# Optimization experiments

Measured on AMD Instinct MI355X. Metric: run time of the kernel, lower is better.

Reference implementation:

```python
import jax, jax.numpy as jnp
import numpy as np

INV_SQRT3 = 1.0 / np.sqrt(3.0)


def setup_inputs() -> dict:
    key = jax.random.key(0)
    ks = jax.random.split(key, 7)
    N = 100000
    M0, M1 = 128, 64  # multiplicities of 0e and 1o irreps in in1 / out
    data_in1 = jax.random.normal(ks[0], (N, M0 + 3 * M1), jnp.float32)  # [N, 320]
    data_in2 = jax.random.normal(ks[1], (N, 1 + 3), jnp.float32)        # [N, 4] = 1x0e + 1x1o
    # e3nn-style path weights, standard normal init (path_normalization='none')
    W00 = jax.random.normal(ks[2], (M0, 1, M0), jnp.float32)  # 0e x 0e -> 0e
    W01 = jax.random.normal(ks[3], (M0, 1, M1), jnp.float32)  # 0e x 1o -> 1o
    W10 = jax.random.normal(ks[4], (M1, 1, M1), jnp.float32)  # 1o x 0e -> 1o
    W11 = jax.random.normal(ks[5], (M1, 1, M0), jnp.float32)  # 1o x 1o -> 0e
    # fan_in of the scalar output slice = 128*1 (0e x 0e) + 64*1 (1o x 1o) = 192
    sqrt_k = 1.0 / np.sqrt(M0 + M1)
    bias = jax.random.uniform(ks[6], (M0,), jnp.float32, -sqrt_k, sqrt_k)
    return {"data_in1": data_in1, "data_in2": data_in2,
            "W00": W00, "W01": W01, "W10": W10, "W11": W11, "bias": bias}


def reference(data_in1, data_in2, W00, W01, W10, W11, bias):
    M0, M1 = W00.shape[0], W10.shape[0]
    N = data_in1.shape[0]
    s1 = data_in1[:, :M0]                      # [N, 128]  scalars 0e
    v1 = data_in1[:, M0:].reshape(N, M1, 3)    # [N, 64, 3] vectors 1o
    s2 = data_in2[:, :1]                       # [N, 1]    scalar attr
    v2 = data_in2[:, 1:].reshape(N, 1, 3)      # [N, 1, 3] vector attr
    # CG paths (component irrep-normalization, path_normalization='none'):
    # wigner-3j folded analytically; net per-path coefs are 1,1,1,1/sqrt(3)
    out0 = jnp.einsum('nu,nv,uvw->nw', s1, s2, W00)                       # 0e x 0e -> 0e
    out0 = out0 + INV_SQRT3 * jnp.einsum('nui,nvi,uvw->nw', v1, v2, W11)  # 1o x 1o -> 0e
    outv = jnp.einsum('nu,nvk,uvw->nwk', s1, v2, W01)                     # 0e x 1o -> 1o
    outv = outv + jnp.einsum('nuk,nv,uvw->nwk', v1, s2, W10)              # 1o x 0e -> 1o
    # indexed bias add: bias_idx selects the l=0 output slice [0:M0]
    out0 = out0 + bias
    return jnp.concatenate([out0, outv.reshape(N, M1 * 3)], axis=1)      # [N, 320]
```

## Files before the change

kernel.cpp:

```cpp
#include <hip/hip_runtime.h>

typedef __bf16 bf16_8 __attribute__((ext_vector_type(8)));
typedef float  f32x4  __attribute__((ext_vector_type(4)));
typedef float  f32x3  __attribute__((ext_vector_type(3), aligned(4)));

#define INV_SQRT3f 0.57735026918962576f


__global__ void tp_convert_weights(
    const float* __restrict__ W00, const float* __restrict__ W01,
    const float* __restrict__ W10, const float* __restrict__ W11,
    __bf16* __restrict__ ws)
{
    const int chunk = blockIdx.x * blockDim.x + threadIdx.x;
    bf16_8 v;
    if (chunk < 2048) {
        const int c = chunk >> 4, q = chunk & 15;
#pragma unroll
        for (int j = 0; j < 8; ++j) v[j] = (__bf16)W00[(q * 8 + j) * 128 + c];
        *(bf16_8*)(ws + (c * 16 + (q ^ (c & 15))) * 8) = v;
    } else if (chunk < 3072) {
        const int idx = chunk - 2048;
        const int c = idx >> 4, q = idx & 15;
#pragma unroll
        for (int j = 0; j < 8; ++j) v[j] = (__bf16)W01[(q * 8 + j) * 64 + c];
        *(bf16_8*)(ws + 16384 + (c * 16 + (q ^ (c & 15))) * 8) = v;
    } else if (chunk < 4096) {
        const int idx = chunk - 3072;
        const int c = idx >> 3, q = idx & 7;
#pragma unroll
        for (int j = 0; j < 8; ++j) v[j] = (__bf16)W11[(q * 8 + j) * 128 + c];
        *(bf16_8*)(ws + 24576 + (c * 8 + (q ^ (c & 7))) * 8) = v;
    } else if (chunk < 4608) {
        const int idx = chunk - 4096;
        const int c = idx >> 3, q = idx & 7;
#pragma unroll
        for (int j = 0; j < 8; ++j) v[j] = (__bf16)W10[(q * 8 + j) * 64 + c];
        *(bf16_8*)(ws + 32768 + idx * 8) = v;
    }
}

__global__ __launch_bounds__(512, 4) void tp_main_kernel(
    const float* __restrict__ din1, const float* __restrict__ din2,
    const __bf16* __restrict__ wsw, const float* __restrict__ bias,
    float* __restrict__ out, int N, int nstrips)
{
    __shared__ __attribute__((aligned(16))) __bf16 smem[32768];
    const __bf16* sw00 = smem;
    const __bf16* sw01 = smem + 16384;
    const __bf16* sw11 = smem + 24576;

    const int tid = threadIdx.x;

    {
        f32x4* d = (f32x4*)smem;
        const f32x4* s = (const f32x4*)wsw;
#pragma unroll
        for (int i = 0; i < 8; ++i)
            d[tid + 512 * i] = s[tid + 512 * i];
    }
    __syncthreads();

    const int wid = (blockIdx.x << 3) + (tid >> 6);
    if (wid < nstrips) {
        const int lane = tid & 63;
        const int mh   = lane & 15;
        const int kq   = lane >> 4;

        int row = wid * 16 + mh;  if (row >= N) row = N - 1;
        const float* __restrict__ r1 = din1 + row * 320;
        const f32x4 d2 = *(const f32x4*)(din2 + row * 4);
        const float s2 = d2.x;

        const __bf16* __restrict__ w10g = wsw + 32768;

        f32x4 accA[8];
        f32x4 accV[3][4];
#pragma unroll
        for (int i = 0; i < 8; ++i) accA[i] = (f32x4)0.0f;
#pragma unroll
        for (int k = 0; k < 3; ++k)
#pragma unroll
            for (int i = 0; i < 4; ++i) accV[k][i] = (f32x4)0.0f;

#pragma unroll
        for (int s = 0; s < 4; ++s) {
            const int off = 32 * s + 8 * kq;
            f32x4 x0 = *(const f32x4*)(r1 + off);
            f32x4 x1 = *(const f32x4*)(r1 + off + 4);
            float xx[8] = {x0.x, x0.y, x0.z, x0.w, x1.x, x1.y, x1.z, x1.w};
            bf16_8 as2, av0, av1, av2;
#pragma unroll
            for (int j = 0; j < 8; ++j) {
                as2[j] = (__bf16)(s2   * xx[j]);
                av0[j] = (__bf16)(d2.y * xx[j]);
                av1[j] = (__bf16)(d2.z * xx[j]);
                av2[j] = (__bf16)(d2.w * xx[j]);
            }
            const int q = 4 * s + kq;
#pragma unroll
            for (int nt = 0; nt < 8; ++nt) {
                const int c = nt * 16 + mh;
                bf16_8 b = *(const bf16_8*)(sw00 + (c * 16 + (q ^ mh)) * 8);
                accA[nt] = __builtin_amdgcn_mfma_f32_16x16x32_bf16(as2, b, accA[nt], 0, 0, 0);
            }
#pragma unroll
            for (int nt = 0; nt < 4; ++nt) {
                const int c = nt * 16 + mh;
                bf16_8 b = *(const bf16_8*)(sw01 + (c * 16 + (q ^ mh)) * 8);
                accV[0][nt] = __builtin_amdgcn_mfma_f32_16x16x32_bf16(av0, b, accV[0][nt], 0, 0, 0);
                accV[1][nt] = __builtin_amdgcn_mfma_f32_16x16x32_bf16(av1, b, accV[1][nt], 0, 0, 0);
                accV[2][nt] = __builtin_amdgcn_mfma_f32_16x16x32_bf16(av2, b, accV[2][nt], 0, 0, 0);
            }
        }

#pragma unroll
        for (int s = 0; s < 2; ++s) {
            const int voff = 128 + 96 * s + 24 * kq;
            float b24[24];
#pragma unroll
            for (int qq = 0; qq < 6; ++qq) {
                f32x4 t4 = *(const f32x4*)(r1 + voff + 4 * qq);
                b24[4 * qq]     = t4.x; b24[4 * qq + 1] = t4.y;
                b24[4 * qq + 2] = t4.z; b24[4 * qq + 3] = t4.w;
            }
            bf16_8 at, ac0, ac1, ac2;
#pragma unroll
            for (int j = 0; j < 8; ++j) {
                const float e0 = b24[3 * j], e1 = b24[3 * j + 1], e2 = b24[3 * j + 2];
                at[j]  = (__bf16)(INV_SQRT3f * (e0 * d2.y + e1 * d2.z + e2 * d2.w));
                ac0[j] = (__bf16)(s2 * e0);
                ac1[j] = (__bf16)(s2 * e1);
                ac2[j] = (__bf16)(s2 * e2);
            }
            const int q = 4 * s + kq;
#pragma unroll
            for (int nt = 0; nt < 8; ++nt) {
                const int c = nt * 16 + mh;
                bf16_8 b = *(const bf16_8*)(sw11 + (c * 8 + (q ^ (mh & 7))) * 8);
                accA[nt] = __builtin_amdgcn_mfma_f32_16x16x32_bf16(at, b, accA[nt], 0, 0, 0);
            }
#pragma unroll
            for (int nt = 0; nt < 4; ++nt) {
                const int c = nt * 16 + mh;
                bf16_8 b = *(const bf16_8*)(w10g + (c * 8 + q) * 8);
                accV[0][nt] = __builtin_amdgcn_mfma_f32_16x16x32_bf16(ac0, b, accV[0][nt], 0, 0, 0);
                accV[1][nt] = __builtin_amdgcn_mfma_f32_16x16x32_bf16(ac1, b, accV[1][nt], 0, 0, 0);
                accV[2][nt] = __builtin_amdgcn_mfma_f32_16x16x32_bf16(ac2, b, accV[2][nt], 0, 0, 0);
            }
        }

        const int rowg0 = wid * 16 + 4 * kq;
#pragma unroll
        for (int nt = 0; nt < 8; ++nt) {
            const float bi = bias[nt * 16 + mh];
#pragma unroll
            for (int r = 0; r < 4; ++r) {
                const int rowg = rowg0 + r;
                if (rowg < N) out[rowg * 320 + nt * 16 + mh] = accA[nt][r] + bi;
            }
        }
#pragma unroll
        for (int r = 0; r < 4; ++r) {
            const int rowg = rowg0 + r;
            if (rowg < N) {
#pragma unroll
                for (int nt = 0; nt < 4; ++nt) {
                    const int w = nt * 16 + mh;
                    f32x3 o;
                    o.x = accV[0][nt][r];
                    o.y = accV[1][nt][r];
                    o.z = accV[2][nt][r];
                    *(f32x3*)(out + rowg * 320 + 128 + 3 * w) = o;
                }
            }
        }
    }
}

extern "C" void kernel_launch(void* const* d_in, const int* in_sizes, int n_in,
                              void* d_out, int out_size, void* d_ws, size_t ws_size,
                              hipStream_t stream)
{
    const float* din1 = (const float*)d_in[0];
    const float* din2 = (const float*)d_in[1];
    const float* W00  = (const float*)d_in[2];
    const float* W01  = (const float*)d_in[3];
    const float* W10  = (const float*)d_in[4];
    const float* W11  = (const float*)d_in[5];
    const float* bias = (const float*)d_in[6];
    float* outp = (float*)d_out;
    __bf16* ws = (__bf16*)d_ws;

    const int N = in_sizes[0] / 320;
    const int nstrips = (N + 15) / 16;
    const int nblocks = (nstrips + 7) / 8;

    hipLaunchKernelGGL(tp_convert_weights, dim3(18), dim3(256), 0, stream,
                       W00, W01, W10, W11, ws);
    hipLaunchKernelGGL(tp_main_kernel, dim3(nblocks), dim3(512), 0, stream,
                       din1, din2, ws, bias, outp, N, nstrips);
}
```

Measured before the change: 283.2 us.

## Make main kernel persistent with register double-buffered prefetch of next strip

The main kernel becomes a persistent grid-stride loop over 16-row strips, capped at 256 blocks. Each block fills LDS with the weights once and then reuses them for many strips, where before every strip-sized block reloaded them. While one strip's MFMA work runs, each wave preloads the next strip's inputs into a second register buffer, aiming to hide global load latency. The cost is much higher register pressure (launch bounds relaxed to 2 blocks) and fewer resident waves. The old clamp of out-of-range rows is gone, so reads past N are possible when N is not a multiple of 16.

```diff
diff --git a/kernel.cpp b/kernel.cpp
--- a/kernel.cpp
+++ b/kernel.cpp
@@ -40,7 +40,126 @@
     }
 }
 
-__global__ __launch_bounds__(512, 4) void tp_main_kernel(
+#define LOAD_S1(P1, D2, S) do {                                               \
+    const float* _r1 = din1 + ((S) * 16 + mh) * 320 + 8 * kq;                 \
+    _Pragma("unroll")                                                         \
+    for (int _t = 0; _t < 4; ++_t) {                                          \
+        P1[2 * _t]     = *(const f32x4*)(_r1 + 32 * _t);                      \
+        P1[2 * _t + 1] = *(const f32x4*)(_r1 + 32 * _t + 4);                  \
+    }                                                                         \
+    D2 = *(const f32x4*)(din2 + ((S) * 16 + mh) * 4);                         \
+} while (0)
+
+#define LOAD_S2(P2, S) do {                                                   \
+    const float* _r2 = din1 + ((S) * 16 + mh) * 320 + 128 + 24 * kq;          \
+    _Pragma("unroll")                                                         \
+    for (int _h = 0; _h < 2; ++_h)                                            \
+        _Pragma("unroll")                                                     \
+        for (int _q = 0; _q < 6; ++_q)                                        \
+            P2[6 * _h + _q] = *(const f32x4*)(_r2 + 96 * _h + 4 * _q);        \
+} while (0)
+
+#define PHASE1(P1, D2) do {                                                   \
+    _Pragma("unroll")                                                         \
+    for (int _i = 0; _i < 8; ++_i) accA[_i] = (f32x4)0.0f;                    \
+    _Pragma("unroll")                                                         \
+    for (int _k = 0; _k < 3; ++_k)                                            \
+        _Pragma("unroll")                                                     \
+        for (int _i = 0; _i < 4; ++_i) accV[_k][_i] = (f32x4)0.0f;            \
+    _Pragma("unroll")                                                         \
+    for (int _s = 0; _s < 4; ++_s) {                                          \
+        const f32x4 _x0 = P1[2 * _s];                                         \
+        const f32x4 _x1 = P1[2 * _s + 1];                                     \
+        float _xx[8] = {_x0.x, _x0.y, _x0.z, _x0.w, _x1.x, _x1.y, _x1.z, _x1.w}; \
+        bf16_8 _as2, _av0, _av1, _av2;                                        \
+        _Pragma("unroll")                                                     \
+        for (int _j = 0; _j < 8; ++_j) {                                      \
+            _as2[_j] = (__bf16)(D2.x * _xx[_j]);                              \
+            _av0[_j] = (__bf16)(D2.y * _xx[_j]);                              \
+            _av1[_j] = (__bf16)(D2.z * _xx[_j]);                              \
+            _av2[_j] = (__bf16)(D2.w * _xx[_j]);                              \
+        }                                                                     \
+        const int _q = 4 * _s + kq;                                           \
+        _Pragma("unroll")                                                     \
+        for (int _nt = 0; _nt < 8; ++_nt) {                                   \
+            const int _c = _nt * 16 + mh;                                     \
+            bf16_8 _b = *(const bf16_8*)(sw00 + (_c * 16 + (_q ^ mh)) * 8);   \
+            accA[_nt] = __builtin_amdgcn_mfma_f32_16x16x32_bf16(_as2, _b, accA[_nt], 0, 0, 0); \
+        }                                                                     \
+        _Pragma("unroll")                                                     \
+        for (int _nt = 0; _nt < 4; ++_nt) {                                   \
+            const int _c = _nt * 16 + mh;                                     \
+            bf16_8 _b = *(const bf16_8*)(sw01 + (_c * 16 + (_q ^ mh)) * 8);   \
+            accV[0][_nt] = __builtin_amdgcn_mfma_f32_16x16x32_bf16(_av0, _b, accV[0][_nt], 0, 0, 0); \
+            accV[1][_nt] = __builtin_amdgcn_mfma_f32_16x16x32_bf16(_av1, _b, accV[1][_nt], 0, 0, 0); \
+            accV[2][_nt] = __builtin_amdgcn_mfma_f32_16x16x32_bf16(_av2, _b, accV[2][_nt], 0, 0, 0); \
+        }                                                                     \
+    }                                                                         \
+} while (0)
+
+#define PHASE2_STORE(P2, D2, S) do {                                          \
+    _Pragma("unroll")                                                         \
+    for (int _s = 0; _s < 2; ++_s) {                                          \
+        float _b24[24];                                                       \
+        _Pragma("unroll")                                                     \
+        for (int _qq = 0; _qq < 6; ++_qq) {                                   \
+            const f32x4 _t4 = P2[6 * _s + _qq];                               \
+            _b24[4 * _qq]     = _t4.x; _b24[4 * _qq + 1] = _t4.y;             \
+            _b24[4 * _qq + 2] = _t4.z; _b24[4 * _qq + 3] = _t4.w;             \
+        }                                                                     \
+        bf16_8 _at, _ac0, _ac1, _ac2;                                         \
+        _Pragma("unroll")                                                     \
+        for (int _j = 0; _j < 8; ++_j) {                                      \
+            const float _e0 = _b24[3 * _j], _e1 = _b24[3 * _j + 1], _e2 = _b24[3 * _j + 2]; \
+            _at[_j]  = (__bf16)(INV_SQRT3f * (_e0 * D2.y + _e1 * D2.z + _e2 * D2.w)); \
+            _ac0[_j] = (__bf16)(D2.x * _e0);                                  \
+            _ac1[_j] = (__bf16)(D2.x * _e1);                                  \
+            _ac2[_j] = (__bf16)(D2.x * _e2);                                  \
+        }                                                                     \
+        const int _q = 4 * _s + kq;                                           \
+        _Pragma("unroll")                                                     \
+        for (int _nt = 0; _nt < 8; ++_nt) {                                   \
+            const int _c = _nt * 16 + mh;                                     \
+            bf16_8 _b = *(const bf16_8*)(sw11 + (_c * 8 + (_q ^ (mh & 7))) * 8); \
+            accA[_nt] = __builtin_amdgcn_mfma_f32_16x16x32_bf16(_at, _b, accA[_nt], 0, 0, 0); \
+        }                                                                     \
+        _Pragma("unroll")                                                     \
+        for (int _nt = 0; _nt < 4; ++_nt) {                                   \
+            const int _c = _nt * 16 + mh;                                     \
+            bf16_8 _b = *(const bf16_8*)(w10g + (_c * 8 + _q) * 8);           \
+            accV[0][_nt] = __builtin_amdgcn_mfma_f32_16x16x32_bf16(_ac0, _b, accV[0][_nt], 0, 0, 0); \
+            accV[1][_nt] = __builtin_amdgcn_mfma_f32_16x16x32_bf16(_ac1, _b, accV[1][_nt], 0, 0, 0); \
+            accV[2][_nt] = __builtin_amdgcn_mfma_f32_16x16x32_bf16(_ac2, _b, accV[2][_nt], 0, 0, 0); \
+        }                                                                     \
+    }                                                                         \
+    const int _rowg0 = (S) * 16 + 4 * kq;                                     \
+    _Pragma("unroll")                                                         \
+    for (int _nt = 0; _nt < 8; ++_nt) {                                       \
+        const float _bi = bias[_nt * 16 + mh];                                \
+        _Pragma("unroll")                                                     \
+        for (int _r = 0; _r < 4; ++_r) {                                      \
+            const int _rowg = _rowg0 + _r;                                    \
+            if (_rowg < N) out[_rowg * 320 + _nt * 16 + mh] = accA[_nt][_r] + _bi; \
+        }                                                                     \
+    }                                                                         \
+    _Pragma("unroll")                                                         \
+    for (int _r = 0; _r < 4; ++_r) {                                          \
+        const int _rowg = _rowg0 + _r;                                        \
+        if (_rowg < N) {                                                      \
+            _Pragma("unroll")                                                 \
+            for (int _nt = 0; _nt < 4; ++_nt) {                               \
+                const int _w = _nt * 16 + mh;                                 \
+                f32x3 _o;                                                     \
+                _o.x = accV[0][_nt][_r];                                      \
+                _o.y = accV[1][_nt][_r];                                      \
+                _o.z = accV[2][_nt][_r];                                      \
+                *(f32x3*)(out + _rowg * 320 + 128 + 3 * _w) = _o;             \
+            }                                                                 \
+        }                                                                     \
+    }                                                                         \
+} while (0)
+
+__global__ __launch_bounds__(512, 2) void tp_main_kernel(
     const float* __restrict__ din1, const float* __restrict__ din2,
     const __bf16* __restrict__ wsw, const float* __restrict__ bias,
     float* __restrict__ out, int N, int nstrips)
@@ -49,130 +168,61 @@
     const __bf16* sw00 = smem;
     const __bf16* sw01 = smem + 16384;
     const __bf16* sw11 = smem + 24576;
-
-    const int tid = threadIdx.x;
+    const __bf16* __restrict__ w10g = wsw + 32768;
+
+    const int tid  = threadIdx.x;
+    const int lane = tid & 63;
+    const int mh   = lane & 15;
+    const int kq   = lane >> 4;
+
+    const int wgid   = (blockIdx.x << 3) + (tid >> 6);
+    const int stride = gridDim.x << 3;
+
+    f32x4 fill[8];
+    {
+        const f32x4* s = (const f32x4*)wsw;
+#pragma unroll
+        for (int i = 0; i < 8; ++i) fill[i] = s[tid + 512 * i];
+    }
+
+    f32x4 p1A[8], p2A[12], d2A;
+    f32x4 p1B[8], p2B[12], d2B;
+    const int s0 = (wgid < nstrips) ? wgid : 0;
+    LOAD_S1(p1A, d2A, s0);
+    LOAD_S2(p2A, s0);
 
     {
         f32x4* d = (f32x4*)smem;
-        const f32x4* s = (const f32x4*)wsw;
-#pragma unroll
-        for (int i = 0; i < 8; ++i)
-            d[tid + 512 * i] = s[tid + 512 * i];
+#pragma unroll
+        for (int i = 0; i < 8; ++i) d[tid + 512 * i] = fill[i];
     }
     __syncthreads();
 
-    const int wid = (blockIdx.x << 3) + (tid >> 6);
-    if (wid < nstrips) {
-        const int lane = tid & 63;
-        const int mh   = lane & 15;
-        const int kq   = lane >> 4;
-
-        int row = wid * 16 + mh;  if (row >= N) row = N - 1;
-        const float* __restrict__ r1 = din1 + row * 320;
-        const f32x4 d2 = *(const f32x4*)(din2 + row * 4);
-        const float s2 = d2.x;
-
-        const __bf16* __restrict__ w10g = wsw + 32768;
-
+    if (wgid < nstrips) {
         f32x4 accA[8];
         f32x4 accV[3][4];
-#pragma unroll
-        for (int i = 0; i < 8; ++i) accA[i] = (f32x4)0.0f;
-#pragma unroll
-        for (int k = 0; k < 3; ++k)
-#pragma unroll
-            for (int i = 0; i < 4; ++i) accV[k][i] = (f32x4)0.0f;
-
-#pragma unroll
-        for (int s = 0; s < 4; ++s) {
-            const int off = 32 * s + 8 * kq;
-            f32x4 x0 = *(const f32x4*)(r1 + off);
-            f32x4 x1 = *(const f32x4*)(r1 + off + 4);
-            float xx[8] = {x0.x, x0.y, x0.z, x0.w, x1.x, x1.y, x1.z, x1.w};
-            bf16_8 as2, av0, av1, av2;
-#pragma unroll
-            for (int j = 0; j < 8; ++j) {
-                as2[j] = (__bf16)(s2   * xx[j]);
-                av0[j] = (__bf16)(d2.y * xx[j]);
-                av1[j] = (__bf16)(d2.z * xx[j]);
-                av2[j] = (__bf16)(d2.w * xx[j]);
+
+        int scur = wgid;
+        while (true) {
+            {
+                const int snxt = scur + stride;
+                const bool has_nxt = snxt < nstrips;
+                if (has_nxt) LOAD_S1(p1B, d2B, snxt);
+                PHASE1(p1A, d2A);
+                if (has_nxt) LOAD_S2(p2B, snxt);
+                PHASE2_STORE(p2A, d2A, scur);
+                if (!has_nxt) break;
+                scur = snxt;
             }
-            const int q = 4 * s + kq;
-#pragma unroll
-            for (int nt = 0; nt < 8; ++nt) {
-                const int c = nt * 16 + mh;
-                bf16_8 b = *(const bf16_8*)(sw00 + (c * 16 + (q ^ mh)) * 8);
-                accA[nt] = __builtin_amdgcn_mfma_f32_16x16x32_bf16(as2, b, accA[nt], 0, 0, 0);
-            }
-#pragma unroll
-            for (int nt = 0; nt < 4; ++nt) {
-                const int c = nt * 16 + mh;
-                bf16_8 b = *(const bf16_8*)(sw01 + (c * 16 + (q ^ mh)) * 8);
-                accV[0][nt] = __builtin_amdgcn_mfma_f32_16x16x32_bf16(av0, b, accV[0][nt], 0, 0, 0);
-                accV[1][nt] = __builtin_amdgcn_mfma_f32_16x16x32_bf16(av1, b, accV[1][nt], 0, 0, 0);
-                accV[2][nt] = __builtin_amdgcn_mfma_f32_16x16x32_bf16(av2, b, accV[2][nt], 0, 0, 0);
-            }
-        }
-
-#pragma unroll
-        for (int s = 0; s < 2; ++s) {
-            const int voff = 128 + 96 * s + 24 * kq;
-            float b24[24];
-#pragma unroll
-            for (int qq = 0; qq < 6; ++qq) {
-                f32x4 t4 = *(const f32x4*)(r1 + voff + 4 * qq);
-                b24[4 * qq]     = t4.x; b24[4 * qq + 1] = t4.y;
-                b24[4 * qq + 2] = t4.z; b24[4 * qq + 3] = t4.w;
-            }
-            bf16_8 at, ac0, ac1, ac2;
-#pragma unroll
-            for (int j = 0; j < 8; ++j) {
-                const float e0 = b24[3 * j], e1 = b24[3 * j + 1], e2 = b24[3 * j + 2];
-                at[j]  = (__bf16)(INV_SQRT3f * (e0 * d2.y + e1 * d2.z + e2 * d2.w));
-                ac0[j] = (__bf16)(s2 * e0);
-                ac1[j] = (__bf16)(s2 * e1);
-                ac2[j] = (__bf16)(s2 * e2);
-            }
-            const int q = 4 * s + kq;
-#pragma unroll
-            for (int nt = 0; nt < 8; ++nt) {
-                const int c = nt * 16 + mh;
-                bf16_8 b = *(const bf16_8*)(sw11 + (c * 8 + (q ^ (mh & 7))) * 8);
-                accA[nt] = __builtin_amdgcn_mfma_f32_16x16x32_bf16(at, b, accA[nt], 0, 0, 0);
-            }
-#pragma unroll
-            for (int nt = 0; nt < 4; ++nt) {
-                const int c = nt * 16 + mh;
-                bf16_8 b = *(const bf16_8*)(w10g + (c * 8 + q) * 8);
-                accV[0][nt] = __builtin_amdgcn_mfma_f32_16x16x32_bf16(ac0, b, accV[0][nt], 0, 0, 0);
-                accV[1][nt] = __builtin_amdgcn_mfma_f32_16x16x32_bf16(ac1, b, accV[1][nt], 0, 0, 0);
-                accV[2][nt] = __builtin_amdgcn_mfma_f32_16x16x32_bf16(ac2, b, accV[2][nt], 0, 0, 0);
-            }
-        }
-
-        const int rowg0 = wid * 16 + 4 * kq;
-#pragma unroll
-        for (int nt = 0; nt < 8; ++nt) {
-            const float bi = bias[nt * 16 + mh];
-#pragma unroll
-            for (int r = 0; r < 4; ++r) {
-                const int rowg = rowg0 + r;
-                if (rowg < N) out[rowg * 320 + nt * 16 + mh] = accA[nt][r] + bi;
-            }
-        }
-#pragma unroll
-        for (int r = 0; r < 4; ++r) {
-            const int rowg = rowg0 + r;
-            if (rowg < N) {
-#pragma unroll
-                for (int nt = 0; nt < 4; ++nt) {
-                    const int w = nt * 16 + mh;
-                    f32x3 o;
-                    o.x = accV[0][nt][r];
-                    o.y = accV[1][nt][r];
-                    o.z = accV[2][nt][r];
-                    *(f32x3*)(out + rowg * 320 + 128 + 3 * w) = o;
-                }
+            {
+                const int snxt = scur + stride;
+                const bool has_nxt = snxt < nstrips;
+                if (has_nxt) LOAD_S1(p1A, d2A, snxt);
+                PHASE1(p1B, d2B);
+                if (has_nxt) LOAD_S2(p2A, snxt);
+                PHASE2_STORE(p2B, d2B, scur);
+                if (!has_nxt) break;
+                scur = snxt;
             }
         }
     }
@@ -194,7 +244,9 @@
 
     const int N = in_sizes[0] / 320;
     const int nstrips = (N + 15) / 16;
-    const int nblocks = (nstrips + 7) / 8;
+
+    int nblocks = 256;
+    if (nblocks * 8 > nstrips) nblocks = (nstrips + 7) / 8;
 
     hipLaunchKernelGGL(tp_convert_weights, dim3(18), dim3(256), 0, stream,
                        W00, W01, W10, W11, ws);
```

After: 427.5 us. 1.51x slower.
